# Optimization experiments

Hardware: AMD Instinct MI355X
Metric: run time of the kernel (lower is better)

## Reference

```python
import jax, jax.numpy as jnp
import numpy as np

B, N, D_IN, D_OUT, T = 2048, 64, 256, 256, 8

def setup_inputs() -> dict:
    key = jax.random.key(0)
    k1, k2, k3, k4, k5 = jax.random.split(key, 5)
    x = jax.random.normal(k1, (B, N, D_IN), dtype=jnp.float32)
    G = jax.random.normal(k2, (N, N), dtype=jnp.float32)
    weight = jax.random.normal(k3, (T, D_OUT, D_IN), dtype=jnp.float32) * (1.0 / np.sqrt(D_IN))
    bias = jax.random.normal(k4, (D_OUT,), dtype=jnp.float32) * 0.01
    node_types = jax.random.randint(k5, (N,), 0, T, dtype=jnp.int64)
    return {"x": x, "G": G, "weight": weight, "bias": bias, "node_types": node_types}

def reference(x, G, weight, bias, node_types):
    # gather per-node weights: (N, out, in)
    w = weight[node_types]
    # per-node matmul: torch gmm(x, w.transpose(-2,-1)) == einsum('noi,bni->bno')
    h = jnp.einsum('noi,bni->bno', w, x)
    # graph influence matmul over node dim, then bias
    out = jnp.einsum('mn,bno->bmo', G, h) + bias
    return out
```

## Files before the change

### kernel.cpp

```cpp
#include <hip/hip_runtime.h>
#include <hip/hip_bf16.h>
#include <cstdint>

#define B_TOT  2048
#define N_NODE 64
#define D_IN   256
#define D_OUT  256
#define N_TYPE 8

typedef __attribute__((ext_vector_type(8))) short bf16x8;
typedef __attribute__((ext_vector_type(4))) float f32x4;
typedef unsigned short u16;

__device__ __forceinline__ u16 f2bf(float f) {
  union { float f; unsigned u; } v; v.f = f;
  unsigned r = v.u + 0x7FFFu + ((v.u >> 16) & 1u);
  return (u16)(r >> 16);
}


__global__ __launch_bounds__(256)
void prep_kernel(const float* __restrict__ w, const float* __restrict__ G,
                 u16* __restrict__ ws)
{
  int e = blockIdx.x * 256 + threadIdx.x;
  if (e < N_TYPE * D_OUT * D_IN) {
    int ty = e >> 16, r = (e >> 8) & 255, k = e & 255;
    int kc = k >> 6, k6 = k & 63;
    int s = (k6 >> 5) * 4 + ((k6 >> 2) & 3);
    int j = ((k6 >> 4) & 1) * 4 + (k6 & 3);
    ws[(size_t)((ty * 4 + kc) * 2048 + r * 8 + (s ^ (r & 7))) * 8 + j] = f2bf(w[e]);
  } else if (e < N_TYPE * D_OUT * D_IN + N_NODE * N_NODE) {
    int g = e - N_TYPE * D_OUT * D_IN;
    int m = g >> 6, n = g & 63;
    int s = (n >> 5) * 4 + ((n >> 2) & 3);
    int j = ((n >> 4) & 1) * 4 + (n & 3);
    ws[524288 + (size_t)(m * 8 + (s ^ (m & 7))) * 8 + j] = f2bf(G[g]);
  }
}

__global__ __launch_bounds__(512, 2)
void pernode_gemm(const float* __restrict__ x, const u16* __restrict__ wimg,
                  const int* __restrict__ types, u16* __restrict__ hout)
{
  const int node  = blockIdx.x & 63;
  const int btile = blockIdx.x >> 6;
  const int b0 = btile * 256;
  const int t = threadIdx.x;
  const int lane = t & 63;
  const int wid = t >> 6;
  const int l15 = lane & 15;
  const int lk  = lane >> 4;
  const int wm  = wid & 3;
  const int wn  = wid >> 2;

  __shared__ u16 lds[4][16384];

  const int ty = types[node];
  const int r  = t >> 1;
  const int hf = t & 1;
  const float* xsrc = x + ((size_t)(b0 + r) * N_NODE + node) * D_IN + hf * 32;
  const u16*   wsrc = wimg + (size_t)ty * 65536 + t * 32;

  f32x4 acc[4][8];
  #pragma unroll
  for (int i = 0; i < 4; ++i)
    #pragma unroll
    for (int j = 0; j < 8; ++j) acc[i][j] = (f32x4){0.f, 0.f, 0.f, 0.f};

  float4 xv[8];
  bf16x8 wv[4];

  #pragma unroll
  for (int i = 0; i < 8; ++i) xv[i] = *(const float4*)(xsrc + i * 4);
  #pragma unroll
  for (int i = 0; i < 4; ++i) wv[i] = *(const bf16x8*)(wsrc + i * 8);
  {
    u16* xd = lds[0]; u16* wd = lds[1];
    #pragma unroll
    for (int u = 0; u < 4; ++u) {
      bf16x8 pv;
      #pragma unroll
      for (int j = 0; j < 8; ++j) {
        int fi = ((j >> 2) << 4) + u * 4 + (j & 3);
        pv[j] = (short)f2bf(((const float*)&xv[fi >> 2])[fi & 3]);
      }
      int s = hf * 4 + u;
      *(bf16x8*)&xd[(size_t)r * 64 + (size_t)(s ^ (r & 7)) * 8] = pv;
    }
    #pragma unroll
    for (int i = 0; i < 4; ++i) *(bf16x8*)&wd[(size_t)t * 32 + i * 8] = wv[i];
  }
  __syncthreads();

  for (int kc = 0; kc < 4; ++kc) {
    const int cur = kc & 1;
    if (kc < 3) {
      #pragma unroll
      for (int i = 0; i < 8; ++i) xv[i] = *(const float4*)(xsrc + (kc + 1) * 64 + i * 4);
      #pragma unroll
      for (int i = 0; i < 4; ++i) wv[i] = *(const bf16x8*)(wsrc + (kc + 1) * 16384 + i * 8);
    }
    const u16* xb = lds[cur * 2];
    const u16* wb = lds[cur * 2 + 1];
    #pragma unroll
    for (int ks = 0; ks < 2; ++ks) {
      bf16x8 af[4];
      #pragma unroll
      for (int m = 0; m < 4; ++m) {
        int row = wm * 64 + m * 16 + l15;
        af[m] = *(const bf16x8*)&xb[(size_t)row * 64 + (size_t)((ks * 4 + lk) ^ (row & 7)) * 8];
      }
      #pragma unroll
      for (int n = 0; n < 8; ++n) {
        int row = wn * 128 + n * 16 + l15;
        bf16x8 bv = *(const bf16x8*)&wb[(size_t)row * 64 + (size_t)((ks * 4 + lk) ^ (row & 7)) * 8];
        #pragma unroll
        for (int m = 0; m < 4; ++m)
          acc[m][n] = __builtin_amdgcn_mfma_f32_16x16x32_bf16(af[m], bv, acc[m][n], 0, 0, 0);
      }
    }
    if (kc < 3) {
      u16* xd = lds[(cur ^ 1) * 2]; u16* wd = lds[(cur ^ 1) * 2 + 1];
      #pragma unroll
      for (int u = 0; u < 4; ++u) {
        bf16x8 pv;
        #pragma unroll
        for (int j = 0; j < 8; ++j) {
          int fi = ((j >> 2) << 4) + u * 4 + (j & 3);
          pv[j] = (short)f2bf(((const float*)&xv[fi >> 2])[fi & 3]);
        }
        int s = hf * 4 + u;
        *(bf16x8*)&xd[(size_t)r * 64 + (size_t)(s ^ (r & 7)) * 8] = pv;
      }
      #pragma unroll
      for (int i = 0; i < 4; ++i) *(bf16x8*)&wd[(size_t)t * 32 + i * 8] = wv[i];
    }
    __syncthreads();
  }

  u16* hl = &lds[0][0];
  #pragma unroll
  for (int m = 0; m < 4; ++m)
    #pragma unroll
    for (int n = 0; n < 8; ++n)
      #pragma unroll
      for (int rr = 0; rr < 4; ++rr) {
        int rowl = wm * 64 + m * 16 + lk * 4 + rr;
        int col  = wn * 128 + n * 16 + l15;
        hl[(size_t)rowl * 256 + (size_t)((col >> 3) ^ (rowl & 31)) * 8 + (col & 7)] =
            f2bf(acc[m][n][rr]);
      }
  __syncthreads();
  u16* dst = hout + (size_t)(b0 + r) * 32768 + node * 256 + hf * 128;
  #pragma unroll
  for (int i = 0; i < 16; ++i) {
    int u = hf * 16 + i;
    bf16x8 v = *(const bf16x8*)&hl[(size_t)r * 256 + (size_t)(u ^ (r & 31)) * 8];
    *(bf16x8*)(dst + i * 8) = v;
  }
}

__global__ __launch_bounds__(256)
void graph_mix(const u16* __restrict__ gimg, const float* __restrict__ bias,
               float* __restrict__ out)
{
  const int b = blockIdx.x;
  const int t = threadIdx.x;
  const int lane = t & 63, wid = t >> 6, l15 = lane & 15, lk = lane >> 4;

  __shared__ u16 himg[16384];
  __shared__ u16 gl[4096];

  const u16* hsrc = (const u16*)((const char*)out + (size_t)b * 65536);
  bf16x8 hv[8], gv[2];
  #pragma unroll
  for (int i = 0; i < 8; ++i) hv[i] = *(const bf16x8*)(hsrc + t * 64 + i * 8);
  #pragma unroll
  for (int i = 0; i < 2; ++i) gv[i] = *(const bf16x8*)(gimg + t * 16 + i * 8);
  float bb[4];
  #pragma unroll
  for (int nt = 0; nt < 4; ++nt) bb[nt] = bias[wid * 64 + nt * 16 + l15];
  #pragma unroll
  for (int i = 0; i < 8; ++i) *(bf16x8*)&himg[t * 64 + i * 8] = hv[i];
  #pragma unroll
  for (int i = 0; i < 2; ++i) *(bf16x8*)&gl[t * 16 + i * 8] = gv[i];
  __syncthreads();

  f32x4 acc[4][4];
  #pragma unroll
  for (int i = 0; i < 4; ++i)
    #pragma unroll
    for (int j = 0; j < 4; ++j) acc[i][j] = (f32x4){0.f, 0.f, 0.f, 0.f};

  #pragma unroll
  for (int ks = 0; ks < 2; ++ks) {
    bf16x8 ag[4];
    #pragma unroll
    for (int mt = 0; mt < 4; ++mt) {
      int row = mt * 16 + l15;
      ag[mt] = *(const bf16x8*)&gl[(size_t)row * 64 + (size_t)((ks * 4 + lk) ^ (row & 7)) * 8];
    }
    #pragma unroll
    for (int nt = 0; nt < 4; ++nt) {
      int o = wid * 64 + nt * 16 + l15;
      bf16x8 bh;
      #pragma unroll
      for (int j = 0; j < 8; ++j) {
        int nk = ks * 32 + lk * 4 + (j & 3) + ((j >> 2) << 4);
        bh[j] = (short)himg[nk * 256 + o];
      }
      #pragma unroll
      for (int mt = 0; mt < 4; ++mt)
        acc[mt][nt] = __builtin_amdgcn_mfma_f32_16x16x32_bf16(ag[mt], bh, acc[mt][nt], 0, 0, 0);
    }
  }
  float* ob = out + (size_t)b * 16384;
  #pragma unroll
  for (int mt = 0; mt < 4; ++mt)
    #pragma unroll
    for (int nt = 0; nt < 4; ++nt)
      #pragma unroll
      for (int rr = 0; rr < 4; ++rr) {
        int m = mt * 16 + lk * 4 + rr;
        int o = wid * 64 + nt * 16 + l15;
        ob[(size_t)m * 256 + o] = acc[mt][nt][rr] + bb[nt];
      }
}

__global__ __launch_bounds__(256)
void pernode_gemm_fb(const float* __restrict__ x, const float* __restrict__ w,
                     const int* __restrict__ types, float* __restrict__ h)
{
  const int node = blockIdx.y;
  const int b0   = blockIdx.x * 64;
  const int t    = threadIdx.x;
  const int lane = t & 63;
  const int wid  = t >> 6;
  const int wm   = wid >> 1;
  const int wn   = wid & 1;
  const int l15  = lane & 15;
  const int lk   = lane >> 4;

  __shared__ alignas(16) u16 xs[64][72];
  __shared__ alignas(16) u16 wsm[256][72];

  const int ty = types[node];
  const float* wb = w + (size_t)ty * (D_OUT * D_IN);
  const float* xb = x + ((size_t)b0 * N_NODE + node) * D_IN;

  f32x4 acc[2][8];
  #pragma unroll
  for (int i = 0; i < 2; ++i)
    #pragma unroll
    for (int j = 0; j < 8; ++j) acc[i][j] = (f32x4){0.f,0.f,0.f,0.f};

  const int cg = t & 15, r0 = t >> 4, c = cg * 4;
  const int dst = (c >> 5) * 32 + ((c >> 2) & 3) * 8 + ((c >> 4) & 1) * 4;

  for (int kc = 0; kc < 4; ++kc) {
    const int k0 = kc * 64;
    #pragma unroll
    for (int p = 0; p < 4; ++p) {
      const int row = r0 + p * 16;
      const float4 v = *(const float4*)(xb + (size_t)row * (N_NODE * D_IN) + k0 + c);
      ushort4 bv = { f2bf(v.x), f2bf(v.y), f2bf(v.z), f2bf(v.w) };
      *(ushort4*)&xs[row][dst] = bv;
    }
    #pragma unroll
    for (int p = 0; p < 16; ++p) {
      const int row = r0 + p * 16;
      const float4 v = *(const float4*)(wb + (size_t)row * D_IN + k0 + c);
      ushort4 bv = { f2bf(v.x), f2bf(v.y), f2bf(v.z), f2bf(v.w) };
      *(ushort4*)&wsm[row][dst] = bv;
    }
    __syncthreads();
    #pragma unroll
    for (int ks = 0; ks < 2; ++ks) {
      bf16x8 af[2], bfv[8];
      #pragma unroll
      for (int tm = 0; tm < 2; ++tm)
        af[tm] = *(const bf16x8*)&xs[wm*32 + tm*16 + l15][ks*32 + lk*8];
      #pragma unroll
      for (int tn = 0; tn < 8; ++tn)
        bfv[tn] = *(const bf16x8*)&wsm[wn*128 + tn*16 + l15][ks*32 + lk*8];
      #pragma unroll
      for (int tm = 0; tm < 2; ++tm)
        #pragma unroll
        for (int tn = 0; tn < 8; ++tn)
          acc[tm][tn] = __builtin_amdgcn_mfma_f32_16x16x32_bf16(af[tm], bfv[tn], acc[tm][tn], 0, 0, 0);
    }
    __syncthreads();
  }
  #pragma unroll
  for (int tm = 0; tm < 2; ++tm)
    #pragma unroll
    for (int tn = 0; tn < 8; ++tn)
      #pragma unroll
      for (int rr = 0; rr < 4; ++rr) {
        const int bb2 = b0 + wm*32 + tm*16 + lk*4 + rr;
        const int oo  = wn*128 + tn*16 + l15;
        h[((size_t)bb2 * N_NODE + node) * D_OUT + oo] = acc[tm][tn][rr];
      }
}

__global__ __launch_bounds__(256)
void graph_mix_fb(const float* __restrict__ G, const float* __restrict__ bias,
                  float* __restrict__ hb)
{
  const int b = blockIdx.x;
  const int t = threadIdx.x;
  float* base = hb + (size_t)b * (N_NODE * D_OUT);
  float hreg[N_NODE];
  #pragma unroll
  for (int n = 0; n < N_NODE; ++n) hreg[n] = base[(size_t)n * D_OUT + t];
  const float bv = bias[t];
  for (int m = 0; m < N_NODE; ++m) {
    const float* gr = G + m * N_NODE;
    float a0 = 0.f, a1 = 0.f, a2 = 0.f, a3 = 0.f;
    #pragma unroll
    for (int n = 0; n < N_NODE; n += 4) {
      a0 += gr[n]     * hreg[n];
      a1 += gr[n + 1] * hreg[n + 1];
      a2 += gr[n + 2] * hreg[n + 2];
      a3 += gr[n + 3] * hreg[n + 3];
    }
    base[(size_t)m * D_OUT + t] = (a0 + a1) + (a2 + a3) + bv;
  }
}

extern "C" void kernel_launch(void* const* d_in, const int* in_sizes, int n_in,
                              void* d_out, int out_size, void* d_ws, size_t ws_size,
                              hipStream_t stream) {
  const float* x     = (const float*)d_in[0];
  const float* G     = (const float*)d_in[1];
  const float* w     = (const float*)d_in[2];
  const float* bias  = (const float*)d_in[3];
  const int*   types = (const int*)d_in[4];

  const size_t WS_NEED = (size_t)(524288 + 4096) * 2;
  if (ws_size >= WS_NEED) {
    u16* ws = (u16*)d_ws;
    prep_kernel<<<2064, 256, 0, stream>>>(w, G, ws);
    pernode_gemm<<<512, 512, 0, stream>>>(x, ws, types, (u16*)d_out);
    graph_mix<<<2048, 256, 0, stream>>>(ws + 524288, bias, (float*)d_out);
  } else {
    dim3 gA(B_TOT / 64, N_NODE);
    pernode_gemm_fb<<<gA, 256, 0, stream>>>(x, w, types, (float*)d_out);
    graph_mix_fb<<<B_TOT, 256, 0, stream>>>(G, bias, (float*)d_out);
  }
}
```

Measured before the change: 102.7 us.

## Load MFMA fragments directly from global memory, dropping LDS staging in per-node GEMM

Rewrites the per-node GEMM so each wave reads its weight and x fragments straight from global memory into registers in MFMA operand layout, removing LDS double buffering, the barriers and the LDS transpose epilogue. The prep kernel changes the weight image to a plain chunked [type][k/32][out][32] layout to match. The output is computed transposed (weights as the A operand) so that results are written directly as 4-element bf16 stores. This removes LDS traffic and synchronization, but gives up cross-wave data reuse, so every wave re-reads x and weights from global or cache with smaller, less coalesced accesses.

```diff
diff --git a/kernel.cpp b/kernel.cpp
--- a/kernel.cpp
+++ b/kernel.cpp
@@ -18,6 +18,14 @@
   return (u16)(r >> 16);
 }
 
+__device__ __forceinline__ bf16x8 cvt8(float4 a, float4 b) {
+  bf16x8 r;
+  r[0] = (short)f2bf(a.x); r[1] = (short)f2bf(a.y);
+  r[2] = (short)f2bf(a.z); r[3] = (short)f2bf(a.w);
+  r[4] = (short)f2bf(b.x); r[5] = (short)f2bf(b.y);
+  r[6] = (short)f2bf(b.z); r[7] = (short)f2bf(b.w);
+  return r;
+}
 
 __global__ __launch_bounds__(256)
 void prep_kernel(const float* __restrict__ w, const float* __restrict__ G,
@@ -25,11 +33,9 @@
 {
   int e = blockIdx.x * 256 + threadIdx.x;
   if (e < N_TYPE * D_OUT * D_IN) {
-    int ty = e >> 16, r = (e >> 8) & 255, k = e & 255;
-    int kc = k >> 6, k6 = k & 63;
-    int s = (k6 >> 5) * 4 + ((k6 >> 2) & 3);
-    int j = ((k6 >> 4) & 1) * 4 + (k6 & 3);
-    ws[(size_t)((ty * 4 + kc) * 2048 + r * 8 + (s ^ (r & 7))) * 8 + j] = f2bf(w[e]);
+    int ty = e >> 16, o = (e >> 8) & 255, k = e & 255;
+    int c = k >> 5, kl = k & 31;
+    ws[(size_t)ty * 65536 + c * 8192 + o * 32 + kl] = f2bf(w[e]);
   } else if (e < N_TYPE * D_OUT * D_IN + N_NODE * N_NODE) {
     int g = e - N_TYPE * D_OUT * D_IN;
     int m = g >> 6, n = g & 63;
@@ -45,22 +51,15 @@
 {
   const int node  = blockIdx.x & 63;
   const int btile = blockIdx.x >> 6;
-  const int b0 = btile * 256;
   const int t = threadIdx.x;
-  const int lane = t & 63;
-  const int wid = t >> 6;
-  const int l15 = lane & 15;
-  const int lk  = lane >> 4;
-  const int wm  = wid & 3;
-  const int wn  = wid >> 2;
-
-  __shared__ u16 lds[4][16384];
+  const int lane = t & 63, wid = t >> 6;
+  const int l15 = lane & 15, lk = lane >> 4;
+  const int o0 = (wid & 3) * 64;
+  const int bb = btile * 256 + (wid >> 2) * 128;
 
   const int ty = types[node];
-  const int r  = t >> 1;
-  const int hf = t & 1;
-  const float* xsrc = x + ((size_t)(b0 + r) * N_NODE + node) * D_IN + hf * 32;
-  const u16*   wsrc = wimg + (size_t)ty * 65536 + t * 32;
+  const u16*   wbp = wimg + (size_t)ty * 65536 + (size_t)(o0 + l15) * 32 + lk * 8;
+  const float* xbp = x + ((size_t)(bb + l15) * N_NODE + node) * D_IN + lk * 8;
 
   f32x4 acc[4][8];
   #pragma unroll
@@ -68,96 +67,37 @@
     #pragma unroll
     for (int j = 0; j < 8; ++j) acc[i][j] = (f32x4){0.f, 0.f, 0.f, 0.f};
 
-  float4 xv[8];
-  bf16x8 wv[4];
-
-  #pragma unroll
-  for (int i = 0; i < 8; ++i) xv[i] = *(const float4*)(xsrc + i * 4);
-  #pragma unroll
-  for (int i = 0; i < 4; ++i) wv[i] = *(const bf16x8*)(wsrc + i * 8);
-  {
-    u16* xd = lds[0]; u16* wd = lds[1];
-    #pragma unroll
-    for (int u = 0; u < 4; ++u) {
-      bf16x8 pv;
-      #pragma unroll
-      for (int j = 0; j < 8; ++j) {
-        int fi = ((j >> 2) << 4) + u * 4 + (j & 3);
-        pv[j] = (short)f2bf(((const float*)&xv[fi >> 2])[fi & 3]);
-      }
-      int s = hf * 4 + u;
-      *(bf16x8*)&xd[(size_t)r * 64 + (size_t)(s ^ (r & 7)) * 8] = pv;
-    }
-    #pragma unroll
-    for (int i = 0; i < 4; ++i) *(bf16x8*)&wd[(size_t)t * 32 + i * 8] = wv[i];
-  }
-  __syncthreads();
-
-  for (int kc = 0; kc < 4; ++kc) {
-    const int cur = kc & 1;
-    if (kc < 3) {
-      #pragma unroll
-      for (int i = 0; i < 8; ++i) xv[i] = *(const float4*)(xsrc + (kc + 1) * 64 + i * 4);
-      #pragma unroll
-      for (int i = 0; i < 4; ++i) wv[i] = *(const bf16x8*)(wsrc + (kc + 1) * 16384 + i * 8);
-    }
-    const u16* xb = lds[cur * 2];
-    const u16* wb = lds[cur * 2 + 1];
-    #pragma unroll
-    for (int ks = 0; ks < 2; ++ks) {
-      bf16x8 af[4];
-      #pragma unroll
-      for (int m = 0; m < 4; ++m) {
-        int row = wm * 64 + m * 16 + l15;
-        af[m] = *(const bf16x8*)&xb[(size_t)row * 64 + (size_t)((ks * 4 + lk) ^ (row & 7)) * 8];
-      }
-      #pragma unroll
-      for (int n = 0; n < 8; ++n) {
-        int row = wn * 128 + n * 16 + l15;
-        bf16x8 bv = *(const bf16x8*)&wb[(size_t)row * 64 + (size_t)((ks * 4 + lk) ^ (row & 7)) * 8];
-        #pragma unroll
-        for (int m = 0; m < 4; ++m)
-          acc[m][n] = __builtin_amdgcn_mfma_f32_16x16x32_bf16(af[m], bv, acc[m][n], 0, 0, 0);
-      }
-    }
-    if (kc < 3) {
-      u16* xd = lds[(cur ^ 1) * 2]; u16* wd = lds[(cur ^ 1) * 2 + 1];
-      #pragma unroll
-      for (int u = 0; u < 4; ++u) {
-        bf16x8 pv;
-        #pragma unroll
-        for (int j = 0; j < 8; ++j) {
-          int fi = ((j >> 2) << 4) + u * 4 + (j & 3);
-          pv[j] = (short)f2bf(((const float*)&xv[fi >> 2])[fi & 3]);
-        }
-        int s = hf * 4 + u;
-        *(bf16x8*)&xd[(size_t)r * 64 + (size_t)(s ^ (r & 7)) * 8] = pv;
-      }
-      #pragma unroll
-      for (int i = 0; i < 4; ++i) *(bf16x8*)&wd[(size_t)t * 32 + i * 8] = wv[i];
-    }
-    __syncthreads();
-  }
-
-  u16* hl = &lds[0][0];
-  #pragma unroll
-  for (int m = 0; m < 4; ++m)
-    #pragma unroll
-    for (int n = 0; n < 8; ++n)
-      #pragma unroll
-      for (int rr = 0; rr < 4; ++rr) {
-        int rowl = wm * 64 + m * 16 + lk * 4 + rr;
-        int col  = wn * 128 + n * 16 + l15;
-        hl[(size_t)rowl * 256 + (size_t)((col >> 3) ^ (rowl & 31)) * 8 + (col & 7)] =
-            f2bf(acc[m][n][rr]);
-      }
-  __syncthreads();
-  u16* dst = hout + (size_t)(b0 + r) * 32768 + node * 256 + hf * 128;
-  #pragma unroll
-  for (int i = 0; i < 16; ++i) {
-    int u = hf * 16 + i;
-    bf16x8 v = *(const bf16x8*)&hl[(size_t)r * 256 + (size_t)(u ^ (r & 31)) * 8];
-    *(bf16x8*)(dst + i * 8) = v;
+  #pragma unroll
+  for (int c = 0; c < 8; ++c) {
+    bf16x8 wf[4];
+    #pragma unroll
+    for (int mf = 0; mf < 4; ++mf)
+      wf[mf] = *(const bf16x8*)(wbp + c * 8192 + mf * 512);
+    float4 xa[8], xc[8];
+    #pragma unroll
+    for (int nf = 0; nf < 8; ++nf) {
+      const float* xp = xbp + (size_t)nf * (16 * N_NODE * D_IN) + c * 32;
+      xa[nf] = *(const float4*)(xp);
+      xc[nf] = *(const float4*)(xp + 4);
+    }
+    #pragma unroll
+    for (int nf = 0; nf < 8; ++nf) {
+      bf16x8 xv = cvt8(xa[nf], xc[nf]);
+      #pragma unroll
+      for (int mf = 0; mf < 4; ++mf)
+        acc[mf][nf] = __builtin_amdgcn_mfma_f32_16x16x32_bf16(wf[mf], xv, acc[mf][nf], 0, 0, 0);
+    }
+  }
+
+  #pragma unroll
+  for (int nf = 0; nf < 8; ++nf) {
+    u16* hp = hout + (size_t)(bb + nf * 16 + l15) * 32768 + node * 256 + o0 + lk * 4;
+    #pragma unroll
+    for (int mf = 0; mf < 4; ++mf) {
+      ushort4 pv = { f2bf(acc[mf][nf][0]), f2bf(acc[mf][nf][1]),
+                     f2bf(acc[mf][nf][2]), f2bf(acc[mf][nf][3]) };
+      *(ushort4*)(hp + mf * 16) = pv;
+    }
   }
 }
 
```

Measured after the change: 125.5 us. 22.2% more time.
